# Kernel optimization log

Measured on AMD Instinct MI355X. Metric: run time of the kernel, lower is better.

## Reference

```python
import jax, jax.numpy as jnp
import numpy as np

# Param packing order: [capacitance_x, capacitance_y] + for each direction in
# (ax, by, xy, yx, xx, yy): [conductance, mean, std, pot]  -> total 26 scalars.
_DIR = {"ax": 0, "by": 1, "xy": 2, "yx": 3, "xx": 4, "yy": 5}

B, T = 4096, 4096


def setup_inputs() -> dict:
    key = jax.random.key(0)
    inputs = jax.random.normal(key, (B, T, 2), dtype=jnp.float32)
    # initializer constants from the keras layer
    params = jnp.asarray([1.0, 1.0] + [0.001, 0.3, 3.0, 1.0] * 6, dtype=jnp.float32)
    return {"inputs": inputs, "params": params}


def reference(inputs, params):
    cap_x, cap_y = params[0], params[1]

    def syn(d, pre, post):
        i = 2 + 4 * _DIR[d]
        g, mean, std, pot = params[i], params[i + 1], params[i + 2], params[i + 3]
        return g * jax.nn.sigmoid(std * (pre - mean)) * (pot - post)

    def step(state, inp):
        x, y = state                      # each [B, 1]
        a, b = inp[:, :1], inp[:, 1:]     # each [B, 1]
        cur_x = syn("ax", a, x) + syn("yx", y, x) + syn("xx", x, x)
        cur_y = syn("by", b, y) + syn("xy", x, y) + syn("yy", y, y)
        x = x + cur_x / cap_x
        y = y + cur_y / cap_y
        out = jnp.concatenate((x, y), axis=-1)  # [B, 2]
        return (x, y), out

    bsz = inputs.shape[0]
    x0 = jnp.zeros((bsz, 1), inputs.dtype)
    y0 = jnp.ones((bsz, 1), inputs.dtype)   # initial state = concat(zeros, ones)
    _, outs = jax.lax.scan(step, (x0, y0), jnp.swapaxes(inputs, 0, 1))  # [T, B, 2]
    return jnp.swapaxes(outs, 0, 1)  # [B, T, 2]
```

## Files before the change

kernel.cpp:

```cpp
#include <hip/hip_runtime.h>

#define TLEN  4096
#define NROWS 4096
#define RPB   32
#define K     32
#define NC    (TLEN / K)
#define LDPAD 66
#define UN    8

__device__ __forceinline__ float fexp2(float x) { return __builtin_amdgcn_exp2f(x); }
__device__ __forceinline__ float frcp(float x)  { return __builtin_amdgcn_rcpf(x); }
__device__ __forceinline__ float sigz(float z)  { return frcp(1.0f + fexp2(z)); }

__device__ __forceinline__ float lane_swap1(float v) {
    int r = __builtin_amdgcn_update_dpp(0, __float_as_int(v), 0xB1, 0xF, 0xF, true);
    return __int_as_float(r);
}

__device__ __forceinline__ void gload_lds16(const float4* g, float4* l) {
    __builtin_amdgcn_global_load_lds((const __attribute__((address_space(1))) void*)g,
                                     (__attribute__((address_space(3))) void*)l,
                                     16, 0, 0);
}
__device__ __forceinline__ void fence_vm0() {
    __builtin_amdgcn_s_waitcnt(0x0f70);
    __builtin_amdgcn_sched_barrier(0);
}

__device__ void run_fast(const float* __restrict__ inp, const float* __restrict__ prm,
                         float* __restrict__ out,
                         float4* __restrict__ ibuf,
                         float* __restrict__ st) {
    const int lane = threadIdx.x;
    const int R0   = blockIdx.x * RPB;
    const int r_   = lane >> 1;
    const int par  = lane & 1;

    const float L2E = 1.4426950408889634f;
    const int inB = par ? 6 : 2, sfB = par ? 22 : 18, t2B = par ? 10 : 14;
    const float ic  = 1.0f / prm[par];
    const float g1  = prm[sfB] * ic, P1 = g1 * prm[sfB + 3], Gn1 = -g1;
    const float g2  = prm[t2B] * ic, P2 = g2 * prm[t2B + 3], Gn2 = -g2;
    const float gA  = prm[inB] * ic, PA = gA * prm[inB + 3], GnA = -gA;
    const float c1i = -prm[inB + 2] * L2E, c0i = prm[inB + 2] * prm[inB + 1] * L2E;
    const float sdz = prm[sfB + 2];
    const float c1s = -sdz * L2E, c0s = sdz * prm[sfB + 1] * L2E;

    float x   = par ? 1.0f : 0.0f;
    float sig = sigz(__builtin_fmaf(c1s, x, c0s));
    float u   = __builtin_fmaf(-sig, sig, sig);
    float q   = 0.5f - sig;

    float2* __restrict__ out2 = (float2*)out;
    float*  wp = st + r_ * LDPAD + par;

    const float4* gbase = (const float4*)inp
                        + (size_t)(R0 + (lane & 31)) * (TLEN / 2) + (lane >> 5);
    auto kick = [&](int c) {
        float4* lb = ibuf + ((c & 1) << 9);
        const float4* gp = gbase + c * 16;
#pragma unroll
        for (int j = 0; j < 8; ++j)
            gload_lds16(gp + 2 * j, lb + (j << 6));
    };

    auto step = [&](float va, int t) {
        float sgin = sigz(__builtin_fmaf(c1i, va, c0i));
        float Av  = __builtin_fmaf(GnA, x, PA);
        float t1v = __builtin_fmaf(Gn1, x, P1);
        float t2v = __builtin_fmaf(Gn2, x, P2);
        float m   = sgin * Av;
        float b2  = __builtin_fmaf(sig, t1v, m);
        float sc  = lane_swap1(sig);
        float dx  = __builtin_fmaf(sc, t2v, b2);
        x = x + dx;
        wp[2 * t] = x;
        float dz  = sdz * dx;
        float tt  = __builtin_fmaf(q, dz, 1.0f);
        float aa  = dz * tt;
        sig = __builtin_fmaf(u, aa, sig);
        u   = __builtin_fmaf(-sig, sig, sig);
        q   = 0.5f - sig;
    };

    kick(0);
    fence_vm0();
    float4 f0 = ibuf[0 * 32 + r_];
    float4 f1 = ibuf[1 * 32 + r_];
    kick(1);

    for (int c = 0; c < NC; ++c) {
        float4* lb = ibuf + ((c & 1) << 9);
#pragma unroll
        for (int tp = 0; tp < 16; ++tp) {
            float4 f = f0; f0 = f1;
            if (tp < 14) f1 = lb[(tp + 2) * 32 + r_];
            step(par ? f.y : f.x, 2 * tp);
            step(par ? f.w : f.z, 2 * tp + 1);
        }
        sig = sigz(__builtin_fmaf(c1s, x, c0s));
        u   = __builtin_fmaf(-sig, sig, sig);
        q   = 0.5f - sig;

        if (c + 1 < NC) {
            fence_vm0();
            float4* ln = ibuf + (((c + 1) & 1) << 9);
            f0 = ln[0 * 32 + r_];
            f1 = ln[1 * 32 + r_];
        }
#pragma unroll
        for (int j = 0; j < 16; ++j) {
            int ro  = 2 * j + (lane >> 5);
            int col = lane & 31;
            float2 v = *(const float2*)&st[ro * LDPAD + col * 2];
            out2[(size_t)(R0 + ro) * TLEN + (size_t)c * K + col] = v;
        }
        if (c + 2 < NC) kick(c + 2);
    }
}

struct LaneConst {
    float c1_in, c0_in, c1_sf, c0_sf, c1_ot, c0_ot;
    float gS_in, gS_cr, gS_sf, gP_in, gP_cr, gP_sf;
};

template<bool SHARED>
__device__ __forceinline__ float do_step_exact(float s, float pre_in, const LaneConst& k) {
    float sig_in = sigz(__builtin_fmaf(k.c1_in, pre_in, k.c0_in));
    float sig_sf = sigz(__builtin_fmaf(k.c1_sf, s, k.c0_sf));
    float sig_ot;
    if (SHARED) sig_ot = sig_sf;
    else        sig_ot = sigz(__builtin_fmaf(k.c1_ot, s, k.c0_ot));
    float sig_cr = lane_swap1(sig_ot);
    float S = __builtin_fmaf(k.gS_in, sig_in, __builtin_fmaf(k.gS_cr, sig_cr, k.gS_sf * sig_sf));
    float P = __builtin_fmaf(k.gP_in, sig_in, __builtin_fmaf(k.gP_cr, sig_cr, k.gP_sf * sig_sf));
    return s + __builtin_fmaf(S, -s, P);
}

template<bool SHARED>
__device__ void run_exact(const float* __restrict__ inp, const float* __restrict__ prm,
                          float* __restrict__ out) {
    const int tid = blockIdx.x * 64 + threadIdx.x;
    const int row = tid >> 1;
    const int par = tid & 1;
    const float L2E = 1.4426950408889634f;
    const int inB = par ? 6 : 2, sfB = par ? 22 : 18, otB = par ? 14 : 10, crB = par ? 10 : 14;
    const float invc = 1.0f / prm[par];
    LaneConst k;
    float sd = prm[inB + 2], mn = prm[inB + 1];
    k.c1_in = -sd * L2E; k.c0_in = sd * mn * L2E;
    sd = prm[sfB + 2]; mn = prm[sfB + 1];
    k.c1_sf = -sd * L2E; k.c0_sf = sd * mn * L2E;
    sd = prm[otB + 2]; mn = prm[otB + 1];
    k.c1_ot = -sd * L2E; k.c0_ot = sd * mn * L2E;
    k.gS_in = prm[inB] * invc; k.gP_in = k.gS_in * prm[inB + 3];
    k.gS_sf = prm[sfB] * invc; k.gP_sf = k.gS_sf * prm[sfB + 3];
    k.gS_cr = prm[crB] * invc; k.gP_cr = k.gS_cr * prm[crB + 3];

    const float4* __restrict__ src = (const float4*)inp + (size_t)row * (TLEN / 2);
    float* __restrict__ dst = out + (size_t)row * (TLEN * 2) + par;
    float s = par ? 1.0f : 0.0f;

    float4 cur[UN], nxt[UN];
#pragma unroll
    for (int j = 0; j < UN; ++j) cur[j] = src[j];
    const int NIT = TLEN / (2 * UN);
    for (int it = 0; it < NIT; ++it) {
        if (it + 1 < NIT) {
#pragma unroll
            for (int j = 0; j < UN; ++j) nxt[j] = src[(it + 1) * UN + j];
        }
        float* dptr = dst + it * (UN * 4);
#pragma unroll
        for (int j = 0; j < UN; ++j) {
            float4 f = cur[j];
            s = do_step_exact<SHARED>(s, par ? f.y : f.x, k);
            dptr[j * 4] = s;
            s = do_step_exact<SHARED>(s, par ? f.w : f.z, k);
            dptr[j * 4 + 2] = s;
        }
#pragma unroll
        for (int j = 0; j < UN; ++j) cur[j] = nxt[j];
    }
}

__global__ __launch_bounds__(64, 1)
void memcell_scan(const float* __restrict__ inp, const float* __restrict__ prm,
                  float* __restrict__ out) {
    __shared__ float4 ibuf[2 * 16 * 32];
    __shared__ float  st[RPB * LDPAD];

    const bool shared = (prm[11] == prm[19]) && (prm[12] == prm[20]) &&
                        (prm[15] == prm[23]) && (prm[16] == prm[24]);
    const float capx = prm[0], capy = prm[1];
    const bool gpos = prm[2] >= 0.f && prm[6] >= 0.f && prm[10] >= 0.f &&
                      prm[14] >= 0.f && prm[18] >= 0.f && prm[22] >= 0.f &&
                      capx > 0.f && capy > 0.f;
    const float sx = (prm[2] + prm[14] + prm[18]) / capx;
    const float sy = (prm[6] + prm[10] + prm[22]) / capy;
    const float lox = fminf(0.f, fminf(prm[5], fminf(prm[17], prm[21])));
    const float hix = fmaxf(0.f, fmaxf(prm[5], fmaxf(prm[17], prm[21])));
    const float loy = fminf(1.f, fminf(prm[9], fminf(prm[13], prm[25])));
    const float hiy = fmaxf(1.f, fmaxf(prm[9], fmaxf(prm[13], prm[25])));
    const float wbx = prm[20] * sx * (hix - lox), wby = prm[24] * sy * (hiy - loy);
    const float zmx = prm[20] * fmaxf(fabsf(lox - prm[19]), fabsf(hix - prm[19]));
    const float zmy = prm[24] * fmaxf(fabsf(loy - prm[23]), fabsf(hiy - prm[23]));
    const bool fast = shared && gpos && sx <= 0.25f && sy <= 0.25f &&
                      wbx <= 0.05f && wby <= 0.05f && zmx <= 20.f && zmy <= 20.f;
    if (fast) {
        run_fast(inp, prm, out, ibuf, st);
    } else {
        if (shared) run_exact<true >(inp, prm, out);
        else        run_exact<false>(inp, prm, out);
    }
}

extern "C" void kernel_launch(void* const* d_in, const int* in_sizes, int n_in,
                              void* d_out, int out_size, void* d_ws, size_t ws_size,
                              hipStream_t stream) {
    (void)in_sizes; (void)n_in; (void)d_ws; (void)ws_size; (void)out_size;
    const float* inp = (const float*)d_in[0];
    const float* prm = (const float*)d_in[1];
    float* out = (float*)d_out;
    memcell_scan<<<dim3(NROWS / RPB), dim3(64), 0, stream>>>(inp, prm, out);
}
```

Baseline: 381.0 us.

## Pack eight independent waves per block and halve the time chunk length

The single-wave block becomes a block of eight waves, each running the fast scan on its own 32 rows with private LDS staging and output buffers. The time chunk shrinks from 32 to 16 steps to fit the larger LDS footprint, and launch bounds now allow two blocks per CU. The aim is more latency hiding per CU. The cost is that the grid drops to 16 blocks, so far fewer CUs are used, and the per-chunk overhead of fences, sigmoid resyncs and stores is paid twice as often.

```diff
diff --git a/kernel.cpp b/kernel.cpp
--- a/kernel.cpp
+++ b/kernel.cpp
@@ -2,10 +2,13 @@
 
 #define TLEN  4096
 #define NROWS 4096
-#define RPB   32
-#define K     32
+#define WPB   8
+#define RPW   32
+#define RPB   (WPB * RPW)
+#define K     16
 #define NC    (TLEN / K)
-#define LDPAD 66
+#define LDPAD 34
+#define IBW   (2 * (K / 2) * 32)
 #define UN    8
 
 __device__ __forceinline__ float fexp2(float x) { return __builtin_amdgcn_exp2f(x); }
@@ -31,8 +34,9 @@
                          float* __restrict__ out,
                          float4* __restrict__ ibuf,
                          float* __restrict__ st) {
-    const int lane = threadIdx.x;
-    const int R0   = blockIdx.x * RPB;
+    const int lane = threadIdx.x & 63;
+    const int wave = threadIdx.x >> 6;
+    const int R0   = blockIdx.x * RPB + wave * RPW;
     const int r_   = lane >> 1;
     const int par  = lane & 1;
 
@@ -57,10 +61,10 @@
     const float4* gbase = (const float4*)inp
                         + (size_t)(R0 + (lane & 31)) * (TLEN / 2) + (lane >> 5);
     auto kick = [&](int c) {
-        float4* lb = ibuf + ((c & 1) << 9);
-        const float4* gp = gbase + c * 16;
-#pragma unroll
-        for (int j = 0; j < 8; ++j)
+        float4* lb = ibuf + ((c & 1) * (IBW / 2));
+        const float4* gp = gbase + c * (K / 2);
+#pragma unroll
+        for (int j = 0; j < K / 4; ++j)
             gload_lds16(gp + 2 * j, lb + (j << 6));
     };
 
@@ -90,11 +94,11 @@
     kick(1);
 
     for (int c = 0; c < NC; ++c) {
-        float4* lb = ibuf + ((c & 1) << 9);
-#pragma unroll
-        for (int tp = 0; tp < 16; ++tp) {
+        float4* lb = ibuf + ((c & 1) * (IBW / 2));
+#pragma unroll
+        for (int tp = 0; tp < K / 2; ++tp) {
             float4 f = f0; f0 = f1;
-            if (tp < 14) f1 = lb[(tp + 2) * 32 + r_];
+            if (tp < K / 2 - 2) f1 = lb[(tp + 2) * 32 + r_];
             step(par ? f.y : f.x, 2 * tp);
             step(par ? f.w : f.z, 2 * tp + 1);
         }
@@ -104,14 +108,14 @@
 
         if (c + 1 < NC) {
             fence_vm0();
-            float4* ln = ibuf + (((c + 1) & 1) << 9);
+            float4* ln = ibuf + (((c + 1) & 1) * (IBW / 2));
             f0 = ln[0 * 32 + r_];
             f1 = ln[1 * 32 + r_];
         }
 #pragma unroll
-        for (int j = 0; j < 16; ++j) {
-            int ro  = 2 * j + (lane >> 5);
-            int col = lane & 31;
+        for (int j = 0; j < 8; ++j) {
+            int ro  = 4 * j + (lane >> 4);
+            int col = lane & 15;
             float2 v = *(const float2*)&st[ro * LDPAD + col * 2];
             out2[(size_t)(R0 + ro) * TLEN + (size_t)c * K + col] = v;
         }
@@ -140,7 +144,7 @@
 template<bool SHARED>
 __device__ void run_exact(const float* __restrict__ inp, const float* __restrict__ prm,
                           float* __restrict__ out) {
-    const int tid = blockIdx.x * 64 + threadIdx.x;
+    const int tid = blockIdx.x * (64 * WPB) + threadIdx.x;
     const int row = tid >> 1;
     const int par = tid & 1;
     const float L2E = 1.4426950408889634f;
@@ -184,11 +188,11 @@
     }
 }
 
-__global__ __launch_bounds__(64, 1)
+__global__ __launch_bounds__(64 * WPB, 2)
 void memcell_scan(const float* __restrict__ inp, const float* __restrict__ prm,
                   float* __restrict__ out) {
-    __shared__ float4 ibuf[2 * 16 * 32];
-    __shared__ float  st[RPB * LDPAD];
+    __shared__ float4 ibuf[WPB * IBW];
+    __shared__ float  st[WPB * RPW * LDPAD];
 
     const bool shared = (prm[11] == prm[19]) && (prm[12] == prm[20]) &&
                         (prm[15] == prm[23]) && (prm[16] == prm[24]);
@@ -208,7 +212,10 @@
     const bool fast = shared && gpos && sx <= 0.25f && sy <= 0.25f &&
                       wbx <= 0.05f && wby <= 0.05f && zmx <= 20.f && zmy <= 20.f;
     if (fast) {
-        run_fast(inp, prm, out, ibuf, st);
+        const int wave = threadIdx.x >> 6;
+        run_fast(inp, prm, out,
+                 ibuf + wave * IBW,
+                 st   + wave * (RPW * LDPAD));
     } else {
         if (shared) run_exact<true >(inp, prm, out);
         else        run_exact<false>(inp, prm, out);
@@ -222,5 +229,5 @@
     const float* inp = (const float*)d_in[0];
     const float* prm = (const float*)d_in[1];
     float* out = (float*)d_out;
-    memcell_scan<<<dim3(NROWS / RPB), dim3(64), 0, stream>>>(inp, prm, out);
-}
+    memcell_scan<<<dim3(NROWS / RPB), dim3(64 * WPB), 0, stream>>>(inp, prm, out);
+}
```

Result: slower. 648.8 us (+70.3%).

## Map one row per lane with both x,y states, halving active blocks

Applied to the files above, without the earlier changes.

The fast path now gives each lane a whole row and carries both the x and y recurrences in one thread, instead of splitting them across lane pairs and exchanging sigmoids through DPP swaps. Each wave covers 64 rows, so only 64 of the 128 launched blocks do work, and the chunk length drops to 16 timesteps with a re-laid-out LDS staging buffer. This removes the cross-lane swap and gives each lane two independent dependency chains to interleave. The cost is that half the CUs sit idle, each lane carries twice the serial work, and smaller chunks mean more frequent fences and stores.

```diff
diff --git a/kernel.cpp b/kernel.cpp
--- a/kernel.cpp
+++ b/kernel.cpp
@@ -2,10 +2,10 @@
 
 #define TLEN  4096
 #define NROWS 4096
-#define RPB   32
-#define K     32
+#define RPW   64
+#define K     16
 #define NC    (TLEN / K)
-#define LDPAD 66
+#define STP   34
 #define UN    8
 
 __device__ __forceinline__ float fexp2(float x) { return __builtin_amdgcn_exp2f(x); }
@@ -32,87 +32,103 @@
                          float4* __restrict__ ibuf,
                          float* __restrict__ st) {
     const int lane = threadIdx.x;
-    const int R0   = blockIdx.x * RPB;
-    const int r_   = lane >> 1;
-    const int par  = lane & 1;
+    const int R0   = blockIdx.x * RPW;
 
     const float L2E = 1.4426950408889634f;
-    const int inB = par ? 6 : 2, sfB = par ? 22 : 18, t2B = par ? 10 : 14;
-    const float ic  = 1.0f / prm[par];
-    const float g1  = prm[sfB] * ic, P1 = g1 * prm[sfB + 3], Gn1 = -g1;
-    const float g2  = prm[t2B] * ic, P2 = g2 * prm[t2B + 3], Gn2 = -g2;
-    const float gA  = prm[inB] * ic, PA = gA * prm[inB + 3], GnA = -gA;
-    const float c1i = -prm[inB + 2] * L2E, c0i = prm[inB + 2] * prm[inB + 1] * L2E;
-    const float sdz = prm[sfB + 2];
-    const float c1s = -sdz * L2E, c0s = sdz * prm[sfB + 1] * L2E;
-
-    float x   = par ? 1.0f : 0.0f;
-    float sig = sigz(__builtin_fmaf(c1s, x, c0s));
-    float u   = __builtin_fmaf(-sig, sig, sig);
-    float q   = 0.5f - sig;
+    const float icx = 1.0f / prm[0];
+    const float g1x = prm[18] * icx, P1x = g1x * prm[21], Gn1x = -g1x;
+    const float g2x = prm[14] * icx, P2x = g2x * prm[17], Gn2x = -g2x;
+    const float gAx = prm[2]  * icx, PAx = gAx * prm[5],  GnAx = -gAx;
+    const float c1ix = -prm[4] * L2E, c0ix = prm[4] * prm[3] * L2E;
+    const float sdzx = prm[20];
+    const float c1sx = -sdzx * L2E, c0sx = sdzx * prm[19] * L2E;
+    const float icy = 1.0f / prm[1];
+    const float g1y = prm[22] * icy, P1y = g1y * prm[25], Gn1y = -g1y;
+    const float g2y = prm[10] * icy, P2y = g2y * prm[13], Gn2y = -g2y;
+    const float gAy = prm[6]  * icy, PAy = gAy * prm[9],  GnAy = -gAy;
+    const float c1iy = -prm[8] * L2E, c0iy = prm[8] * prm[7] * L2E;
+    const float sdzy = prm[24];
+    const float c1sy = -sdzy * L2E, c0sy = sdzy * prm[23] * L2E;
+
+    float x = 0.0f, y = 1.0f;
+    float sgX = sigz(__builtin_fmaf(c1sx, x, c0sx));
+    float sgY = sigz(__builtin_fmaf(c1sy, y, c0sy));
+    float uX  = __builtin_fmaf(-sgX, sgX, sgX), qX = 0.5f - sgX;
+    float uY  = __builtin_fmaf(-sgY, sgY, sgY), qY = 0.5f - sgY;
 
     float2* __restrict__ out2 = (float2*)out;
-    float*  wp = st + r_ * LDPAD + par;
-
-    const float4* gbase = (const float4*)inp
-                        + (size_t)(R0 + (lane & 31)) * (TLEN / 2) + (lane >> 5);
+    float*  wp = st + lane * STP;
+
+    const float4* gbase = (const float4*)inp + (size_t)(R0 + lane) * (TLEN / 2);
     auto kick = [&](int c) {
         float4* lb = ibuf + ((c & 1) << 9);
-        const float4* gp = gbase + c * 16;
-#pragma unroll
-        for (int j = 0; j < 8; ++j)
-            gload_lds16(gp + 2 * j, lb + (j << 6));
+        const float4* gp = gbase + c * (K / 2);
+#pragma unroll
+        for (int j = 0; j < K / 2; ++j)
+            gload_lds16(gp + j, lb + (j << 6));
     };
 
-    auto step = [&](float va, int t) {
-        float sgin = sigz(__builtin_fmaf(c1i, va, c0i));
-        float Av  = __builtin_fmaf(GnA, x, PA);
-        float t1v = __builtin_fmaf(Gn1, x, P1);
-        float t2v = __builtin_fmaf(Gn2, x, P2);
-        float m   = sgin * Av;
-        float b2  = __builtin_fmaf(sig, t1v, m);
-        float sc  = lane_swap1(sig);
-        float dx  = __builtin_fmaf(sc, t2v, b2);
-        x = x + dx;
-        wp[2 * t] = x;
-        float dz  = sdz * dx;
-        float tt  = __builtin_fmaf(q, dz, 1.0f);
-        float aa  = dz * tt;
-        sig = __builtin_fmaf(u, aa, sig);
-        u   = __builtin_fmaf(-sig, sig, sig);
-        q   = 0.5f - sig;
+    auto step2 = [&](float a, float b, int t) {
+        float sA  = sigz(__builtin_fmaf(c1ix, a, c0ix));
+        float sB  = sigz(__builtin_fmaf(c1iy, b, c0iy));
+        float AvX = __builtin_fmaf(GnAx, x, PAx);
+        float t1X = __builtin_fmaf(Gn1x, x, P1x);
+        float t2X = __builtin_fmaf(Gn2x, x, P2x);
+        float AvY = __builtin_fmaf(GnAy, y, PAy);
+        float t1Y = __builtin_fmaf(Gn1y, y, P1y);
+        float t2Y = __builtin_fmaf(Gn2y, y, P2y);
+        float mX  = sA * AvX,                mY  = sB * AvY;
+        float b2X = __builtin_fmaf(sgX, t1X, mX);
+        float b2Y = __builtin_fmaf(sgY, t1Y, mY);
+        float dX  = __builtin_fmaf(sgY, t2X, b2X);
+        float dY  = __builtin_fmaf(sgX, t2Y, b2Y);
+        x = x + dX;
+        y = y + dY;
+        float2 w; w.x = x; w.y = y;
+        *(float2*)&wp[2 * t] = w;
+        float dzX = sdzx * dX,               dzY = sdzy * dY;
+        float ttX = __builtin_fmaf(qX, dzX, 1.0f);
+        float ttY = __builtin_fmaf(qY, dzY, 1.0f);
+        float aaX = dzX * ttX,               aaY = dzY * ttY;
+        sgX = __builtin_fmaf(uX, aaX, sgX);
+        sgY = __builtin_fmaf(uY, aaY, sgY);
+        uX  = __builtin_fmaf(-sgX, sgX, sgX);
+        uY  = __builtin_fmaf(-sgY, sgY, sgY);
+        qX  = 0.5f - sgX;
+        qY  = 0.5f - sgY;
     };
 
     kick(0);
     fence_vm0();
-    float4 f0 = ibuf[0 * 32 + r_];
-    float4 f1 = ibuf[1 * 32 + r_];
+    float4 f0 = ibuf[lane];
+    float4 f1 = ibuf[64 + lane];
     kick(1);
 
     for (int c = 0; c < NC; ++c) {
         float4* lb = ibuf + ((c & 1) << 9);
 #pragma unroll
-        for (int tp = 0; tp < 16; ++tp) {
+        for (int tp = 0; tp < K / 2; ++tp) {
             float4 f = f0; f0 = f1;
-            if (tp < 14) f1 = lb[(tp + 2) * 32 + r_];
-            step(par ? f.y : f.x, 2 * tp);
-            step(par ? f.w : f.z, 2 * tp + 1);
-        }
-        sig = sigz(__builtin_fmaf(c1s, x, c0s));
-        u   = __builtin_fmaf(-sig, sig, sig);
-        q   = 0.5f - sig;
+            if (tp < K / 2 - 2) f1 = lb[(tp + 2) * 64 + lane];
+            step2(f.x, f.y, 2 * tp);
+            step2(f.z, f.w, 2 * tp + 1);
+        }
+        sgX = sigz(__builtin_fmaf(c1sx, x, c0sx));
+        uX  = __builtin_fmaf(-sgX, sgX, sgX); qX = 0.5f - sgX;
+        sgY = sigz(__builtin_fmaf(c1sy, y, c0sy));
+        uY  = __builtin_fmaf(-sgY, sgY, sgY); qY = 0.5f - sgY;
 
         if (c + 1 < NC) {
             fence_vm0();
             float4* ln = ibuf + (((c + 1) & 1) << 9);
-            f0 = ln[0 * 32 + r_];
-            f1 = ln[1 * 32 + r_];
+            f0 = ln[lane];
+            f1 = ln[64 + lane];
         }
 #pragma unroll
         for (int j = 0; j < 16; ++j) {
-            int ro  = 2 * j + (lane >> 5);
-            int col = lane & 31;
-            float2 v = *(const float2*)&st[ro * LDPAD + col * 2];
+            int ro  = 4 * j + (lane >> 4);
+            int col = lane & 15;
+            float2 v = *(const float2*)&st[ro * STP + 2 * col];
             out2[(size_t)(R0 + ro) * TLEN + (size_t)c * K + col] = v;
         }
         if (c + 2 < NC) kick(c + 2);
@@ -187,8 +203,8 @@
 __global__ __launch_bounds__(64, 1)
 void memcell_scan(const float* __restrict__ inp, const float* __restrict__ prm,
                   float* __restrict__ out) {
-    __shared__ float4 ibuf[2 * 16 * 32];
-    __shared__ float  st[RPB * LDPAD];
+    __shared__ float4 ibuf[2 * (K / 2) * 64];
+    __shared__ float  st[RPW * STP];
 
     const bool shared = (prm[11] == prm[19]) && (prm[12] == prm[20]) &&
                         (prm[15] == prm[23]) && (prm[16] == prm[24]);
@@ -208,7 +224,8 @@
     const bool fast = shared && gpos && sx <= 0.25f && sy <= 0.25f &&
                       wbx <= 0.05f && wby <= 0.05f && zmx <= 20.f && zmy <= 20.f;
     if (fast) {
-        run_fast(inp, prm, out, ibuf, st);
+        if (blockIdx.x < NROWS / RPW)
+            run_fast(inp, prm, out, ibuf, st);
     } else {
         if (shared) run_exact<true >(inp, prm, out);
         else        run_exact<false>(inp, prm, out);
@@ -222,5 +239,5 @@
     const float* inp = (const float*)d_in[0];
     const float* prm = (const float*)d_in[1];
     float* out = (float*)d_out;
-    memcell_scan<<<dim3(NROWS / RPB), dim3(64), 0, stream>>>(inp, prm, out);
-}
+    memcell_scan<<<dim3(128), dim3(64), 0, stream>>>(inp, prm, out);
+}
```

Result: slower. 570.7 us (+49.8%).

## Specialize a producer wave for input sigmoids, loads and output flushes

Applied to the files above, without the earlier changes.

The block now holds two waves. One wave loads inputs from global memory, computes the input-synapse sigmoids into a double-buffered LDS slab, and writes finished output chunks back to global memory. The other wave runs only the serial recurrence, reading precomputed sigmoids from LDS. This takes transcendental work and store traffic off the latency-bound recurrence wave. The cost is a block-wide barrier per 32-step chunk and twice the LDS footprint for the double-buffered state and sigmoid slabs; the exact fallback path is adapted to the 128-thread block.

```diff
diff --git a/kernel.cpp b/kernel.cpp
--- a/kernel.cpp
+++ b/kernel.cpp
@@ -6,6 +6,8 @@
 #define K     32
 #define NC    (TLEN / K)
 #define LDPAD 66
+#define SGSL  (16 * 32)
+#define STSL  (RPB * LDPAD)
 #define UN    8
 
 __device__ __forceinline__ float fexp2(float x) { return __builtin_amdgcn_exp2f(x); }
@@ -17,105 +19,108 @@
     return __int_as_float(r);
 }
 
-__device__ __forceinline__ void gload_lds16(const float4* g, float4* l) {
-    __builtin_amdgcn_global_load_lds((const __attribute__((address_space(1))) void*)g,
-                                     (__attribute__((address_space(3))) void*)l,
-                                     16, 0, 0);
-}
-__device__ __forceinline__ void fence_vm0() {
-    __builtin_amdgcn_s_waitcnt(0x0f70);
-    __builtin_amdgcn_sched_barrier(0);
-}
-
 __device__ void run_fast(const float* __restrict__ inp, const float* __restrict__ prm,
                          float* __restrict__ out,
-                         float4* __restrict__ ibuf,
-                         float* __restrict__ st) {
-    const int lane = threadIdx.x;
+                         float4* __restrict__ sgbuf,
+                         float*  __restrict__ st) {
+    const int tid  = threadIdx.x;
+    const int wid  = tid >> 6;
+    const int lane = tid & 63;
     const int R0   = blockIdx.x * RPB;
-    const int r_   = lane >> 1;
-    const int par  = lane & 1;
-
     const float L2E = 1.4426950408889634f;
-    const int inB = par ? 6 : 2, sfB = par ? 22 : 18, t2B = par ? 10 : 14;
-    const float ic  = 1.0f / prm[par];
-    const float g1  = prm[sfB] * ic, P1 = g1 * prm[sfB + 3], Gn1 = -g1;
-    const float g2  = prm[t2B] * ic, P2 = g2 * prm[t2B + 3], Gn2 = -g2;
-    const float gA  = prm[inB] * ic, PA = gA * prm[inB + 3], GnA = -gA;
-    const float c1i = -prm[inB + 2] * L2E, c0i = prm[inB + 2] * prm[inB + 1] * L2E;
-    const float sdz = prm[sfB + 2];
-    const float c1s = -sdz * L2E, c0s = sdz * prm[sfB + 1] * L2E;
-
-    float x   = par ? 1.0f : 0.0f;
-    float sig = sigz(__builtin_fmaf(c1s, x, c0s));
-    float u   = __builtin_fmaf(-sig, sig, sig);
-    float q   = 0.5f - sig;
-
     float2* __restrict__ out2 = (float2*)out;
-    float*  wp = st + r_ * LDPAD + par;
-
-    const float4* gbase = (const float4*)inp
-                        + (size_t)(R0 + (lane & 31)) * (TLEN / 2) + (lane >> 5);
-    auto kick = [&](int c) {
-        float4* lb = ibuf + ((c & 1) << 9);
-        const float4* gp = gbase + c * 16;
-#pragma unroll
-        for (int j = 0; j < 8; ++j)
-            gload_lds16(gp + 2 * j, lb + (j << 6));
-    };
-
-    auto step = [&](float va, int t) {
-        float sgin = sigz(__builtin_fmaf(c1i, va, c0i));
-        float Av  = __builtin_fmaf(GnA, x, PA);
-        float t1v = __builtin_fmaf(Gn1, x, P1);
-        float t2v = __builtin_fmaf(Gn2, x, P2);
-        float m   = sgin * Av;
-        float b2  = __builtin_fmaf(sig, t1v, m);
-        float sc  = lane_swap1(sig);
-        float dx  = __builtin_fmaf(sc, t2v, b2);
-        x = x + dx;
-        wp[2 * t] = x;
-        float dz  = sdz * dx;
-        float tt  = __builtin_fmaf(q, dz, 1.0f);
-        float aa  = dz * tt;
-        sig = __builtin_fmaf(u, aa, sig);
-        u   = __builtin_fmaf(-sig, sig, sig);
-        q   = 0.5f - sig;
-    };
-
-    kick(0);
-    fence_vm0();
-    float4 f0 = ibuf[0 * 32 + r_];
-    float4 f1 = ibuf[1 * 32 + r_];
-    kick(1);
-
-    for (int c = 0; c < NC; ++c) {
-        float4* lb = ibuf + ((c & 1) << 9);
-#pragma unroll
-        for (int tp = 0; tp < 16; ++tp) {
-            float4 f = f0; f0 = f1;
-            if (tp < 14) f1 = lb[(tp + 2) * 32 + r_];
-            step(par ? f.y : f.x, 2 * tp);
-            step(par ? f.w : f.z, 2 * tp + 1);
-        }
-        sig = sigz(__builtin_fmaf(c1s, x, c0s));
-        u   = __builtin_fmaf(-sig, sig, sig);
-        q   = 0.5f - sig;
-
-        if (c + 1 < NC) {
-            fence_vm0();
-            float4* ln = ibuf + (((c + 1) & 1) << 9);
-            f0 = ln[0 * 32 + r_];
-            f1 = ln[1 * 32 + r_];
-        }
-#pragma unroll
-        for (int j = 0; j < 16; ++j) {
-            int ro  = 2 * j + (lane >> 5);
-            int col = lane & 31;
-            float2 v = *(const float2*)&st[ro * LDPAD + col * 2];
-            out2[(size_t)(R0 + ro) * TLEN + (size_t)c * K + col] = v;
-        }
-        if (c + 2 < NC) kick(c + 2);
+
+    if (wid == 1) {
+        const int r = lane & 31, h = lane >> 5;
+        const float c1x = -prm[4] * L2E, c0x = prm[4] * prm[3] * L2E;
+        const float c1y = -prm[8] * L2E, c0y = prm[8] * prm[7] * L2E;
+        const float4* __restrict__ src = (const float4*)inp + (size_t)(R0 + r) * (TLEN / 2);
+
+        auto produce = [&](int c) {
+            float4* sl = sgbuf + ((c & 1) ? SGSL : 0);
+            const int base = c * 16 + h * 8;
+#pragma unroll
+            for (int j = 0; j < 8; ++j) {
+                float4 v = src[base + j];
+                float4 o;
+                o.x = sigz(__builtin_fmaf(c1x, v.x, c0x));
+                o.y = sigz(__builtin_fmaf(c1y, v.y, c0y));
+                o.z = sigz(__builtin_fmaf(c1x, v.z, c0x));
+                o.w = sigz(__builtin_fmaf(c1y, v.w, c0y));
+                sl[(h * 8 + j) * 32 + r] = o;
+            }
+        };
+        auto flush = [&](int c) {
+            const float* sl = st + ((c & 1) ? STSL : 0);
+            const int col = lane & 31;
+#pragma unroll
+            for (int j = 0; j < 16; ++j) {
+                int ro = 2 * j + (lane >> 5);
+                float2 v = *(const float2*)&sl[ro * LDPAD + col * 2];
+                out2[(size_t)(R0 + ro) * TLEN + (size_t)c * K + col] = v;
+            }
+        };
+
+        produce(0);
+        __syncthreads();
+        for (int c = 0; c < NC; ++c) {
+            if (c + 1 < NC) produce(c + 1);
+            if (c >= 1)     flush(c - 1);
+            __syncthreads();
+        }
+        flush(NC - 1);
+    } else {
+        const int r_  = lane >> 1;
+        const int par = lane & 1;
+        const int inB = par ? 6 : 2, sfB = par ? 22 : 18, t2B = par ? 10 : 14;
+        const float ic  = 1.0f / prm[par];
+        const float g1  = prm[sfB] * ic, P1 = g1 * prm[sfB + 3], Gn1 = -g1;
+        const float g2  = prm[t2B] * ic, P2 = g2 * prm[t2B + 3], Gn2 = -g2;
+        const float gA  = prm[inB] * ic, PA = gA * prm[inB + 3], GnA = -gA;
+        const float sdz = prm[sfB + 2];
+        const float c1s = -sdz * L2E, c0s = sdz * prm[sfB + 1] * L2E;
+
+        float x   = par ? 1.0f : 0.0f;
+        float sig = sigz(__builtin_fmaf(c1s, x, c0s));
+        float u   = __builtin_fmaf(-sig, sig, sig);
+        float q   = 0.5f - sig;
+
+        auto step = [&](float sg, float* wp, int t) {
+            float Av  = __builtin_fmaf(GnA, x, PA);
+            float t1v = __builtin_fmaf(Gn1, x, P1);
+            float t2v = __builtin_fmaf(Gn2, x, P2);
+            float m   = sg * Av;
+            float b2  = __builtin_fmaf(sig, t1v, m);
+            float sc  = lane_swap1(sig);
+            float dx  = __builtin_fmaf(sc, t2v, b2);
+            x = x + dx;
+            wp[2 * t] = x;
+            float dz = sdz * dx;
+            float tt = __builtin_fmaf(q, dz, 1.0f);
+            float aa = dz * tt;
+            sig = __builtin_fmaf(u, aa, sig);
+            u   = __builtin_fmaf(-sig, sig, sig);
+            q   = 0.5f - sig;
+        };
+
+        __syncthreads();
+        for (int c = 0; c < NC; ++c) {
+            const float4* lb = sgbuf + ((c & 1) ? SGSL : 0);
+            float* wp = st + ((c & 1) ? STSL : 0) + r_ * LDPAD + par;
+            float4 f0 = lb[r_];
+            float4 f1 = lb[32 + r_];
+#pragma unroll
+            for (int tp = 0; tp < 16; ++tp) {
+                float4 f = f0; f0 = f1;
+                if (tp < 14) f1 = lb[(tp + 2) * 32 + r_];
+                step(par ? f.y : f.x, wp, 2 * tp);
+                step(par ? f.w : f.z, wp, 2 * tp + 1);
+            }
+            sig = sigz(__builtin_fmaf(c1s, x, c0s));
+            u   = __builtin_fmaf(-sig, sig, sig);
+            q   = 0.5f - sig;
+            __syncthreads();
+        }
     }
 }
 
@@ -140,8 +145,9 @@
 template<bool SHARED>
 __device__ void run_exact(const float* __restrict__ inp, const float* __restrict__ prm,
                           float* __restrict__ out) {
-    const int tid = blockIdx.x * 64 + threadIdx.x;
+    const int tid = blockIdx.x * 128 + threadIdx.x;
     const int row = tid >> 1;
+    if (row >= NROWS) return;
     const int par = tid & 1;
     const float L2E = 1.4426950408889634f;
     const int inB = par ? 6 : 2, sfB = par ? 22 : 18, otB = par ? 14 : 10, crB = par ? 10 : 14;
@@ -184,11 +190,11 @@
     }
 }
 
-__global__ __launch_bounds__(64, 1)
+__global__ __launch_bounds__(128, 1)
 void memcell_scan(const float* __restrict__ inp, const float* __restrict__ prm,
                   float* __restrict__ out) {
-    __shared__ float4 ibuf[2 * 16 * 32];
-    __shared__ float  st[RPB * LDPAD];
+    __shared__ float4 sgbuf[2 * SGSL];
+    __shared__ float  st[2 * STSL];
 
     const bool shared = (prm[11] == prm[19]) && (prm[12] == prm[20]) &&
                         (prm[15] == prm[23]) && (prm[16] == prm[24]);
@@ -208,7 +214,7 @@
     const bool fast = shared && gpos && sx <= 0.25f && sy <= 0.25f &&
                       wbx <= 0.05f && wby <= 0.05f && zmx <= 20.f && zmy <= 20.f;
     if (fast) {
-        run_fast(inp, prm, out, ibuf, st);
+        run_fast(inp, prm, out, sgbuf, st);
     } else {
         if (shared) run_exact<true >(inp, prm, out);
         else        run_exact<false>(inp, prm, out);
@@ -222,5 +228,5 @@
     const float* inp = (const float*)d_in[0];
     const float* prm = (const float*)d_in[1];
     float* out = (float*)d_out;
-    memcell_scan<<<dim3(NROWS / RPB), dim3(64), 0, stream>>>(inp, prm, out);
-}
+    memcell_scan<<<dim3(NROWS / RPB), dim3(128), 0, stream>>>(inp, prm, out);
+}
```

Result: faster. 351.3 us (-7.8%).
